# Optimization experiments

Measured on AMD Instinct MI355X. Metric: run time of the kernel, lower is better.

Reference implementation:

```python
import jax, jax.numpy as jnp
import numpy as np

N, F, K_KEEP = 4096, 256, 2048

def setup_inputs() -> dict:
    key = jax.random.key(0)
    k1, k2, k3, k4 = jax.random.split(key, 4)
    X = jax.random.normal(k1, (N, F), dtype=jnp.float32)
    A = jax.random.uniform(k2, (N, N), dtype=jnp.float32)
    S = jnp.sort(jax.random.randint(k3, (N,), 0, 16).astype(jnp.int64))
    kernel = jax.random.normal(k4, (F, 1), dtype=jnp.float32) * (1.0 / np.sqrt(F))
    return {"X": X, "A": A, "S": S, "kernel": kernel}

def reference(X, A, S, kernel):
    # score projection with L2-normalized kernel (normalized over all elements)
    kn = kernel / jnp.sqrt(jnp.sum(kernel * kernel))
    y = X @ kn                                   # (N, 1)
    # top-k node selection; boolean_mask via scatter preserves index order,
    # so gather with sorted indices is exactly equivalent
    _, idx = jax.lax.top_k(y[:, 0], K_KEEP)
    idx = jnp.sort(idx)                          # (k,)
    features = X * jnp.tanh(y)                   # (N, F)
    X_pooled = features[idx]                     # (k, F)
    A2 = A @ A                                   # (N, N) -- preserves connectivity
    A_pooled = A2[idx][:, idx]                   # (k, k)
    S_pooled = S[idx]                            # (k,)
    return X_pooled, A_pooled, S_pooled
```

## Files before the change

### kernel.cpp

```cpp
#include <hip/hip_runtime.h>
#include <hip/hip_bf16.h>


#define NN 4096
#define FF 256
#define KKEEP 2048
#define KDIM 4096

typedef __attribute__((ext_vector_type(8))) short short8;
typedef __attribute__((ext_vector_type(4))) float f32x4;

__device__ __forceinline__ unsigned short f2bf(float x) {
  unsigned u = __float_as_uint(x);
  unsigned r = (u + 0x7FFFu + ((u >> 16) & 1u)) >> 16;
  return (unsigned short)r;
}

__device__ __forceinline__ void gload_lds16(const void* g, void* l) {
  __builtin_amdgcn_global_load_lds((const __attribute__((address_space(1))) void*)g,
                                   (__attribute__((address_space(3))) void*)l, 16, 0, 0);
}

__global__ __launch_bounds__(256) void k_score(const float* __restrict__ X,
                                               const float* __restrict__ kern,
                                               float* __restrict__ y) {
  int t = threadIdx.x, lane = t & 63, w = t >> 6;
  int row = blockIdx.x * 4 + w;
  const float4* X4 = (const float4*)(X + (size_t)row * FF);
  const float4* K4 = (const float4*)kern;
  float4 xv = X4[lane];
  float4 kv = K4[lane];
  float p  = xv.x * kv.x + xv.y * kv.y + xv.z * kv.z + xv.w * kv.w;
  float pk = kv.x * kv.x + kv.y * kv.y + kv.z * kv.z + kv.w * kv.w;
  #pragma unroll
  for (int off = 32; off; off >>= 1) {
    p  += __shfl_xor(p, off);
    pk += __shfl_xor(pk, off);
  }
  if (lane == 0) y[row] = p / sqrtf(pk);
}

__global__ __launch_bounds__(256) void k_rank(const float* __restrict__ y,
                                              int* __restrict__ sel) {
  __shared__ __align__(16) float ys[NN];
  __shared__ int part[4][16];
  int t = threadIdx.x;
  const float4* Y4 = (const float4*)y;
  float4* ys4 = (float4*)ys;
  #pragma unroll
  for (int k = 0; k < 4; ++k) ys4[t + k * 256] = Y4[t + k * 256];
  __syncthreads();
  int lane = t & 63, w = t >> 6;
  int r = lane & 15;
  int i = blockIdx.x * 16 + r;
  int seg = w * 4 + (lane >> 4);
  float yi = ys[i];
  int cnt = 0;
  #pragma unroll 4
  for (int s = 0; s < 64; ++s) {
    int f4 = seg * 64 + ((s + seg * 4) & 63);
    float4 v = ys4[f4];
    int j = f4 * 4;
    cnt += (int)((v.x > yi) || (v.x == yi && (j + 0) < i));
    cnt += (int)((v.y > yi) || (v.y == yi && (j + 1) < i));
    cnt += (int)((v.z > yi) || (v.z == yi && (j + 2) < i));
    cnt += (int)((v.w > yi) || (v.w == yi && (j + 3) < i));
  }
  cnt += __shfl_xor(cnt, 16);
  cnt += __shfl_xor(cnt, 32);
  if (lane < 16) part[w][lane] = cnt;
  __syncthreads();
  if (w == 0 && lane < 16) {
    int tot = part[0][lane] + part[1][lane] + part[2][lane] + part[3][lane];
    sel[blockIdx.x * 16 + lane] = (tot < KKEEP) ? 1 : 0;
  }
}

__global__ __launch_bounds__(256) void k_compact(const int* __restrict__ sel,
                                                 const int* __restrict__ S32,
                                                 int* __restrict__ idxb,
                                                 float* __restrict__ outSf,
                                                 long long* __restrict__ outSi,
                                                 int smode) {
  __shared__ int sums[256];
  __shared__ int offs[256];
  int t = threadIdx.x;
  int base = t * 16;
  int loc[16];
  int s = 0;
  #pragma unroll
  for (int u = 0; u < 16; ++u) { loc[u] = sel[base + u]; s += loc[u]; }
  sums[t] = s;
  __syncthreads();
  if (t == 0) {
    int acc = 0;
    for (int q = 0; q < 256; ++q) { offs[q] = acc; acc += sums[q]; }
  }
  __syncthreads();
  bool in64 = (S32[NN - 1] == 0);
  int pos = offs[t];
  for (int u = 0; u < 16; ++u) {
    if (loc[u]) {
      int gi = base + u;
      idxb[pos] = gi;
      int sval = in64 ? S32[2 * gi] : S32[gi];
      if (smode == 0) outSf[pos] = (float)sval;
      else            outSi[pos] = (long long)sval;
      ++pos;
    }
  }
}

__global__ __launch_bounds__(256) void k_gatherAX(const float* __restrict__ A,
                                                  const float* __restrict__ X,
                                                  const float* __restrict__ y,
                                                  const int* __restrict__ idxb,
                                                  unsigned short* __restrict__ Ag,
                                                  float* __restrict__ outX) {
  int tid = blockIdx.x * 256 + threadIdx.x;
  #pragma unroll
  for (int it = 0; it < 8; ++it) {
    int e = tid + it * 262144;
    int p = e >> 10, c4 = e & 1023;
    int r = idxb[p];
    float4 v = ((const float4*)(A + (size_t)r * NN))[c4];
    ushort4 o;
    o.x = f2bf(v.x); o.y = f2bf(v.y); o.z = f2bf(v.z); o.w = f2bf(v.w);
    ((ushort4*)Ag)[e] = o;
  }
  if (tid < 131072) {
    int p = tid >> 6, c4 = tid & 63;
    int r = idxb[p];
    float ty = tanhf(y[r]);
    float4 v = ((const float4*)(X + (size_t)r * FF))[c4];
    v.x *= ty; v.y *= ty; v.z *= ty; v.w *= ty;
    ((float4*)outX)[tid] = v;
  }
}

__global__ __launch_bounds__(256) void k_packB(const float* __restrict__ A,
                                               const int* __restrict__ idxb,
                                               unsigned short* __restrict__ Bt) {
  __shared__ unsigned short tile[64][66];
  __shared__ int sidx[64];
  int t = threadIdx.x;
  int bk = blockIdx.x & 63;
  int bq = blockIdx.x >> 6;
  int k0 = bk * 64, q0 = bq * 64;
  if (t < 64) sidx[t] = idxb[q0 + t];
  __syncthreads();
  int j = t & 63, i0 = t >> 6;
  #pragma unroll
  for (int rr = 0; rr < 16; ++rr) {
    int i = i0 + rr * 4;
    float v = A[(size_t)(k0 + i) * NN + sidx[j]];
    tile[i][j] = f2bf(v);
  }
  __syncthreads();
  int i2 = t & 63, j0 = t >> 6;
  #pragma unroll
  for (int rr = 0; rr < 16; ++rr) {
    int jj = j0 + rr * 4;
    Bt[(size_t)(q0 + jj) * KDIM + k0 + i2] = tile[i2][jj];
  }
}

__global__ __launch_bounds__(256) void k_gemm(const unsigned short* __restrict__ Ag,
                                              const unsigned short* __restrict__ Bt,
                                              float* __restrict__ Cdst, int kseg) {
  __shared__ __align__(16) unsigned short lA[128 * 32];
  __shared__ __align__(16) unsigned short lB[128 * 32];
  int t = threadIdx.x, lane = t & 63, w = t >> 6;
  int bx = blockIdx.x, by = blockIdx.y, s = blockIdx.z;
  int wm = w >> 1, wn = w & 1;
  int fr = lane & 15, fq = lane >> 4;
  f32x4 zero = {0.f, 0.f, 0.f, 0.f};
  f32x4 acc[4][4];
  #pragma unroll
  for (int mf = 0; mf < 4; ++mf)
    #pragma unroll
    for (int nf = 0; nf < 4; ++nf) acc[mf][nf] = zero;

  int kbeg = s * kseg, kend = kbeg + kseg;
  for (int k0 = kbeg; k0 < kend; k0 += 32) {
    #pragma unroll
    for (int jj = 0; jj < 2; ++jj) {
      int chunk = jj * 4 + w;
      int e = chunk * 64 + lane;
      int r = e >> 2, kk = (e & 3) * 8;
      gload_lds16(Ag + (size_t)(by * 128 + r) * KDIM + k0 + kk, lA + chunk * 512);
      gload_lds16(Bt + (size_t)(bx * 128 + r) * KDIM + k0 + kk, lB + chunk * 512);
    }
    __syncthreads();
    short8 a[4], b[4];
    #pragma unroll
    for (int mf = 0; mf < 4; ++mf)
      a[mf] = *(const short8*)&lA[(wm * 64 + mf * 16 + fr) * 32 + fq * 8];
    #pragma unroll
    for (int nf = 0; nf < 4; ++nf)
      b[nf] = *(const short8*)&lB[(wn * 64 + nf * 16 + fr) * 32 + fq * 8];
    #pragma unroll
    for (int mf = 0; mf < 4; ++mf)
      #pragma unroll
      for (int nf = 0; nf < 4; ++nf)
        acc[mf][nf] = __builtin_amdgcn_mfma_f32_16x16x32_bf16(a[mf], b[nf], acc[mf][nf], 0, 0, 0);
    __syncthreads();
  }
  float* Cp = Cdst + (size_t)s * KKEEP * KKEEP;
  #pragma unroll
  for (int mf = 0; mf < 4; ++mf)
    #pragma unroll
    for (int nf = 0; nf < 4; ++nf)
      #pragma unroll
      for (int r = 0; r < 4; ++r) {
        int row = by * 128 + wm * 64 + mf * 16 + fq * 4 + r;
        int col = bx * 128 + wn * 64 + nf * 16 + fr;
        Cp[(size_t)row * KKEEP + col] = acc[mf][nf][r];
      }
}

__global__ __launch_bounds__(256) void k_reduce(const float* __restrict__ Cpart,
                                                float* __restrict__ outA, int nsplit) {
  const size_t Q = (size_t)KKEEP * KKEEP / 4;
  size_t e = (size_t)blockIdx.x * 256 + threadIdx.x;
  const float4* P = (const float4*)Cpart;
  float4 o = P[e];
  for (int s = 1; s < nsplit; ++s) {
    float4 v = P[e + (size_t)s * Q];
    o.x += v.x; o.y += v.y; o.z += v.z; o.w += v.w;
  }
  ((float4*)outA)[e] = o;
}

extern "C" void kernel_launch(void* const* d_in, const int* in_sizes, int n_in,
                              void* d_out, int out_size, void* d_ws, size_t ws_size,
                              hipStream_t stream) {
  const float* X    = (const float*)d_in[0];
  const float* A    = (const float*)d_in[1];
  const int*   S32  = (const int*)d_in[2];
  const float* kern = (const float*)d_in[3];

  float* out  = (float*)d_out;
  float* outX = out;
  float* outA = out + 2048 * 256;
  float*      outSf = out + 2048 * 256 + 2048 * 2048;
  long long*  outSi = (long long*)((char*)d_out + (size_t)(2048 * 256 + 2048 * 2048) * 4);
  int smode = (out_size == 4722688) ? 1 : 0;

  char* wsb = (char*)d_ws;
  float* y    = (float*)wsb;
  int*   sel  = (int*)(wsb + 16384);
  int*   idxb = (int*)(wsb + 32768);
  unsigned short* Ag = (unsigned short*)(wsb + 65536);
  unsigned short* Bt = Ag + (size_t)KKEEP * KDIM;
  float* Cpart = (float*)(Bt + (size_t)KKEEP * KDIM);

  const size_t PART = (size_t)KKEEP * KKEEP * 4;
  const size_t BASE = 65536 + (size_t)KKEEP * KDIM * 2 * 2;
  int ksplit = 1;
  if (ws_size >= BASE + 4 * PART)      ksplit = 4;
  else if (ws_size >= BASE + 2 * PART) ksplit = 2;
  float* gemmDst = (ksplit > 1) ? Cpart : outA;

  hipLaunchKernelGGL(k_score,    dim3(1024),  dim3(256), 0, stream, X, kern, y);
  hipLaunchKernelGGL(k_rank,     dim3(256),   dim3(256), 0, stream, y, sel);
  hipLaunchKernelGGL(k_compact,  dim3(1),     dim3(256), 0, stream, sel, S32, idxb, outSf, outSi, smode);
  hipLaunchKernelGGL(k_gatherAX, dim3(1024),  dim3(256), 0, stream, A, X, y, idxb, Ag, outX);
  hipLaunchKernelGGL(k_packB,    dim3(2048),  dim3(256), 0, stream, A, idxb, Bt);
  hipLaunchKernelGGL(k_gemm,     dim3(16, 16, ksplit), dim3(256), 0, stream,
                     Ag, Bt, gemmDst, KDIM / ksplit);
  if (ksplit > 1)
    hipLaunchKernelGGL(k_reduce, dim3(4096),  dim3(256), 0, stream, Cpart, outA, ksplit);
}
```

Before: 216.8 us.

## Rewrite GEMM with 256x128 tiles, triple-buffered LDS pipeline and swizzle

Replaces the 128x128, BK=32 single-buffered GEMM with a 512-thread 256x128x64 tile kernel. It uses a three-stage LDS ring fed by direct global-to-LDS loads and waits on vmcnt so loads overlap MFMA work. It also XOR-swizzles LDS rows to avoid bank conflicts, raises wave priority around the MFMA block, and lowers the split-K to at most 2 to cut partial-sum traffic in the reduce. The larger tiles mean fewer CTAs, which risks lower occupancy and load imbalance, and the swizzle and vmcnt accounting must be exactly right.

```diff
diff --git a/kernel.cpp b/kernel.cpp
--- a/kernel.cpp
+++ b/kernel.cpp
@@ -6,6 +6,11 @@
 #define FF 256
 #define KKEEP 2048
 #define KDIM 4096
+
+#define BM 256
+#define BN 128
+#define BK 64
+#define LDSBUF 49152
 
 typedef __attribute__((ext_vector_type(8))) short short8;
 typedef __attribute__((ext_vector_type(4))) float f32x4;
@@ -165,57 +170,109 @@
   }
 }
 
-__global__ __launch_bounds__(256) void k_gemm(const unsigned short* __restrict__ Ag,
-                                              const unsigned short* __restrict__ Bt,
-                                              float* __restrict__ Cdst, int kseg) {
-  __shared__ __align__(16) unsigned short lA[128 * 32];
-  __shared__ __align__(16) unsigned short lB[128 * 32];
+__device__ __forceinline__ void stage_rows(const unsigned short* __restrict__ srcbase,
+                                           int rowoff, int koff,
+                                           char* ldsregion, int j, int t, int w) {
+  int p = j * 8192 + t * 16;
+  int row = p >> 7;
+  int l = p ^ ((row & 7) << 4);
+  const unsigned short* src = srcbase + (size_t)(rowoff + row) * KDIM + koff + ((l & 127) >> 1);
+  gload_lds16(src, ldsregion + j * 8192 + w * 1024);
+}
+
+__global__ __launch_bounds__(512, 2) void k_gemm2(const unsigned short* __restrict__ Ag,
+                                                  const unsigned short* __restrict__ Bt,
+                                                  float* __restrict__ Cdst, int nt) {
+  __shared__ __align__(16) unsigned short lds[3 * LDSBUF / 2];
   int t = threadIdx.x, lane = t & 63, w = t >> 6;
-  int bx = blockIdx.x, by = blockIdx.y, s = blockIdx.z;
+  int bx = blockIdx.x, by = blockIdx.y, z = blockIdx.z;
   int wm = w >> 1, wn = w & 1;
   int fr = lane & 15, fq = lane >> 4;
-  f32x4 zero = {0.f, 0.f, 0.f, 0.f};
+  int kbase = z * nt * BK;
+
   f32x4 acc[4][4];
   #pragma unroll
   for (int mf = 0; mf < 4; ++mf)
     #pragma unroll
-    for (int nf = 0; nf < 4; ++nf) acc[mf][nf] = zero;
-
-  int kbeg = s * kseg, kend = kbeg + kseg;
-  for (int k0 = kbeg; k0 < kend; k0 += 32) {
+    for (int nf = 0; nf < 4; ++nf) acc[mf][nf] = f32x4{0.f, 0.f, 0.f, 0.f};
+
+  #pragma unroll
+  for (int pt = 0; pt < 2; ++pt) {
+    char* bufA = (char*)lds + pt * LDSBUF;
+    char* bufB = bufA + 32768;
+    int koff = kbase + pt * BK;
+    stage_rows(Ag, by * BM, koff, bufA, 0, t, w);
+    stage_rows(Ag, by * BM, koff, bufA, 1, t, w);
+    stage_rows(Ag, by * BM, koff, bufA, 2, t, w);
+    stage_rows(Ag, by * BM, koff, bufA, 3, t, w);
+    stage_rows(Bt, bx * BN, koff, bufB, 0, t, w);
+    stage_rows(Bt, bx * BN, koff, bufB, 1, t, w);
+  }
+
+  int cb = 0;
+  for (int kt = 0; kt < nt; ++kt) {
+    if (kt == nt - 1) asm volatile("s_waitcnt vmcnt(0)" ::: "memory");
+    else              asm volatile("s_waitcnt vmcnt(6)" ::: "memory");
+    __builtin_amdgcn_s_barrier();
+
+    int sb = cb + 2; if (sb >= 3) sb -= 3;
+    const char* lA = (const char*)lds + cb * LDSBUF;
+    const char* lB = lA + 32768;
+    char* sA = (char*)lds + sb * LDSBUF;
+    char* sB = sA + 32768;
+    bool doStage = (kt + 2) < nt;
+    int koff2 = kbase + (kt + 2) * BK;
+
     #pragma unroll
-    for (int jj = 0; jj < 2; ++jj) {
-      int chunk = jj * 4 + w;
-      int e = chunk * 64 + lane;
-      int r = e >> 2, kk = (e & 3) * 8;
-      gload_lds16(Ag + (size_t)(by * 128 + r) * KDIM + k0 + kk, lA + chunk * 512);
-      gload_lds16(Bt + (size_t)(bx * 128 + r) * KDIM + k0 + kk, lB + chunk * 512);
+    for (int ksub = 0; ksub < 2; ++ksub) {
+      if (doStage) {
+        if (ksub == 0) {
+          stage_rows(Ag, by * BM, koff2, sA, 0, t, w);
+          stage_rows(Ag, by * BM, koff2, sA, 1, t, w);
+          stage_rows(Ag, by * BM, koff2, sA, 2, t, w);
+        } else {
+          stage_rows(Ag, by * BM, koff2, sA, 3, t, w);
+          stage_rows(Bt, bx * BN, koff2, sB, 0, t, w);
+          stage_rows(Bt, bx * BN, koff2, sB, 1, t, w);
+        }
+      }
+      short8 a[4], b[4];
+      #pragma unroll
+      for (int mf = 0; mf < 4; ++mf) {
+        int r = wm * 64 + mf * 16 + fr;
+        int lb = r * 128 + ksub * 64 + fq * 16;
+        int pb = lb ^ ((r & 7) << 4);
+        a[mf] = *(const short8*)(lA + pb);
+      }
+      #pragma unroll
+      for (int nf = 0; nf < 4; ++nf) {
+        int r = wn * 64 + nf * 16 + fr;
+        int lb = r * 128 + ksub * 64 + fq * 16;
+        int pb = lb ^ ((r & 7) << 4);
+        b[nf] = *(const short8*)(lB + pb);
+      }
+      __builtin_amdgcn_s_setprio(1);
+      #pragma unroll
+      for (int mf = 0; mf < 4; ++mf)
+        #pragma unroll
+        for (int nf = 0; nf < 4; ++nf)
+          acc[mf][nf] = __builtin_amdgcn_mfma_f32_16x16x32_bf16(a[mf], b[nf], acc[mf][nf], 0, 0, 0);
+      __builtin_amdgcn_s_setprio(0);
     }
-    __syncthreads();
-    short8 a[4], b[4];
-    #pragma unroll
-    for (int mf = 0; mf < 4; ++mf)
-      a[mf] = *(const short8*)&lA[(wm * 64 + mf * 16 + fr) * 32 + fq * 8];
-    #pragma unroll
-    for (int nf = 0; nf < 4; ++nf)
-      b[nf] = *(const short8*)&lB[(wn * 64 + nf * 16 + fr) * 32 + fq * 8];
-    #pragma unroll
-    for (int mf = 0; mf < 4; ++mf)
-      #pragma unroll
-      for (int nf = 0; nf < 4; ++nf)
-        acc[mf][nf] = __builtin_amdgcn_mfma_f32_16x16x32_bf16(a[mf], b[nf], acc[mf][nf], 0, 0, 0);
-    __syncthreads();
-  }
-  float* Cp = Cdst + (size_t)s * KKEEP * KKEEP;
+    __builtin_amdgcn_s_barrier();
+    cb = (cb + 1 == 3) ? 0 : cb + 1;
+  }
+
+  float* Cp = Cdst + (size_t)z * KKEEP * KKEEP;
   #pragma unroll
   for (int mf = 0; mf < 4; ++mf)
     #pragma unroll
     for (int nf = 0; nf < 4; ++nf)
       #pragma unroll
-      for (int r = 0; r < 4; ++r) {
-        int row = by * 128 + wm * 64 + mf * 16 + fq * 4 + r;
-        int col = bx * 128 + wn * 64 + nf * 16 + fr;
-        Cp[(size_t)row * KKEEP + col] = acc[mf][nf][r];
+      for (int rr = 0; rr < 4; ++rr) {
+        int row = by * BM + wm * 64 + mf * 16 + fq * 4 + rr;
+        int col = bx * BN + wn * 64 + nf * 16 + fr;
+        Cp[(size_t)row * KKEEP + col] = acc[mf][nf][rr];
       }
 }
 
@@ -257,18 +314,17 @@
 
   const size_t PART = (size_t)KKEEP * KKEEP * 4;
   const size_t BASE = 65536 + (size_t)KKEEP * KDIM * 2 * 2;
-  int ksplit = 1;
-  if (ws_size >= BASE + 4 * PART)      ksplit = 4;
-  else if (ws_size >= BASE + 2 * PART) ksplit = 2;
+  int ksplit = (ws_size >= BASE + 2 * PART) ? 2 : 1;
   float* gemmDst = (ksplit > 1) ? Cpart : outA;
+  int nt = KDIM / (BK * ksplit);
 
   hipLaunchKernelGGL(k_score,    dim3(1024),  dim3(256), 0, stream, X, kern, y);
   hipLaunchKernelGGL(k_rank,     dim3(256),   dim3(256), 0, stream, y, sel);
   hipLaunchKernelGGL(k_compact,  dim3(1),     dim3(256), 0, stream, sel, S32, idxb, outSf, outSi, smode);
   hipLaunchKernelGGL(k_gatherAX, dim3(1024),  dim3(256), 0, stream, A, X, y, idxb, Ag, outX);
   hipLaunchKernelGGL(k_packB,    dim3(2048),  dim3(256), 0, stream, A, idxb, Bt);
-  hipLaunchKernelGGL(k_gemm,     dim3(16, 16, ksplit), dim3(256), 0, stream,
-                     Ag, Bt, gemmDst, KDIM / ksplit);
+  hipLaunchKernelGGL(k_gemm2,    dim3(16, 8, ksplit), dim3(512), 0, stream,
+                     Ag, Bt, gemmDst, nt);
   if (ksplit > 1)
     hipLaunchKernelGGL(k_reduce, dim3(4096),  dim3(256), 0, stream, Cpart, outA, ksplit);
 }
```

After: 186.2 us. 1.16x faster.
